# Kernel optimization log

Measured on AMD Instinct MI355X. Metric: run time of the kernel, lower is better.

Reference implementation:

```python
import jax, jax.numpy as jnp
import numpy as np

B, T, DM, H, D = 4, 2048, 1024, 16, 64
INNER = H * D


def setup_inputs() -> dict:
    key = jax.random.key(0)
    ks = jax.random.split(key, 8)
    s = 0.02
    x = jax.random.normal(ks[0], (B, T, DM), dtype=jnp.float32)
    state = jnp.zeros((B, H, D, D), dtype=jnp.float32)
    Wq = jax.random.normal(ks[1], (DM, INNER), dtype=jnp.float32) * s
    Wk = jax.random.normal(ks[2], (DM, INNER), dtype=jnp.float32) * s
    Wv = jax.random.normal(ks[3], (DM, INNER), dtype=jnp.float32) * s
    Wa = jax.random.normal(ks[4], (DM, H), dtype=jnp.float32) * s
    ba = jnp.zeros((H,), dtype=jnp.float32)
    Wb = jax.random.normal(ks[5], (DM, H), dtype=jnp.float32) * s
    bb = jnp.zeros((H,), dtype=jnp.float32)  # beta_init=0.5 -> logit(0.5)=0
    Wo = jax.random.normal(ks[6], (INNER, DM), dtype=jnp.float32) * s
    return {"x": x, "state": state, "Wq": Wq, "Wk": Wk, "Wv": Wv,
            "Wa": Wa, "ba": ba, "Wb": Wb, "bb": bb, "Wo": Wo}


def reference(x, state, Wq, Wk, Wv, Wa, ba, Wb, bb, Wo):
    Bb, Tt, _ = x.shape
    Q = (x @ Wq).reshape(Bb, Tt, H, D)
    K = (x @ Wk).reshape(Bb, Tt, H, D)
    V = (x @ Wv).reshape(Bb, Tt, H, D)
    alpha = jax.nn.sigmoid(x @ Wa + ba)  # (B,T,H) forget gate
    beta = jax.nn.sigmoid(x @ Wb + bb)   # (B,T,H) write gate
    # F.normalize(p=2, dim=-1) with eps=1e-12 clamp on the norm
    K = K / jnp.maximum(jnp.linalg.norm(K, axis=-1, keepdims=True), 1e-12)

    def step(S, inp):
        qt, kt, vt, at, bt = inp  # (B,H,D),(B,H,D),(B,H,D),(B,H),(B,H)
        S = at[..., None, None] * S + bt[..., None, None] * jnp.einsum('bhi,bhj->bhij', vt, kt)
        yt = jnp.einsum('bhij,bhj->bhi', S, qt)
        return S, yt

    xs = (jnp.swapaxes(Q, 0, 1), jnp.swapaxes(K, 0, 1), jnp.swapaxes(V, 0, 1),
          jnp.swapaxes(alpha, 0, 1), jnp.swapaxes(beta, 0, 1))
    S, ys = jax.lax.scan(step, state, xs)  # ys: (T,B,H,D)
    out = jnp.swapaxes(ys, 0, 1).reshape(Bb, Tt, INNER) @ Wo
    return out, S
```

## Files before the change

### kernel.cpp

```cpp
#include <hip/hip_runtime.h>
#include <hip/hip_bf16.h>
#include <math.h>

#define B_SZ   4
#define T_LEN  2048
#define DM     1024
#define NH     16
#define DH     64
#define INNER  1024
#define NROWS  (B_SZ*T_LEN)
#define NQ     (NROWS*INNER)
#define CH     64
#define NCH    (T_LEN/CH)

typedef __bf16 bf16x8 __attribute__((ext_vector_type(8)));
typedef __bf16 bf16x4 __attribute__((ext_vector_type(4)));
typedef float  f32x4  __attribute__((ext_vector_type(4)));
typedef __attribute__((address_space(3))) void*       lds_vp;
typedef const __attribute__((address_space(1))) void* gbl_vp;

__device__ __forceinline__ int swz(int row, int col) {
    return (row << 6) + ((((col >> 3) + (row >> 2)) & 7) << 3) + (col & 7);
}

__global__ __launch_bounds__(256) void wt_cast_transpose(const float* __restrict__ Wq,
                                                         const float* __restrict__ Wk,
                                                         const float* __restrict__ Wv,
                                                         const float* __restrict__ Wo,
                                                         __bf16* __restrict__ WqT,
                                                         __bf16* __restrict__ WkT,
                                                         __bf16* __restrict__ WvT,
                                                         __bf16* __restrict__ WoT) {
    __shared__ float tile[64][65];
    const float* W;
    __bf16* WT;
    if      (blockIdx.z == 0) { W = Wq; WT = WqT; }
    else if (blockIdx.z == 1) { W = Wk; WT = WkT; }
    else if (blockIdx.z == 2) { W = Wv; WT = WvT; }
    else                      { W = Wo; WT = WoT; }

    const int k0 = blockIdx.y * 64, n0 = blockIdx.x * 64;
    const int tr  = threadIdx.x >> 4;
    const int tc4 = (threadIdx.x & 15) * 4;

#pragma unroll
    for (int r = 0; r < 4; r++) {
        const int k = tr + 16 * r;
        const float4 v = *(const float4*)(W + (size_t)(k0 + k) * DM + n0 + tc4);
        tile[k][tc4 + 0] = v.x;
        tile[k][tc4 + 1] = v.y;
        tile[k][tc4 + 2] = v.z;
        tile[k][tc4 + 3] = v.w;
    }
    __syncthreads();
#pragma unroll
    for (int r = 0; r < 4; r++) {
        const int n = tr + 16 * r;
        bf16x4 o;
#pragma unroll
        for (int j = 0; j < 4; j++) o[j] = (__bf16)tile[tc4 + j][n];
        *(bf16x4*)(WT + (size_t)(n0 + n) * DM + k0 + tc4) = o;
    }
}

#define STAGE_STRIDE 24576
#define B_BASE 16384

template <typename CT>
__device__ __forceinline__ void gemm_pipe_body(const __bf16* __restrict__ A,
                                               const __bf16* __restrict__ BT,
                                               CT* __restrict__ C,
                                               int m0, int n0bt, int n0c) {
    __shared__ __align__(16) char lds[3 * STAGE_STRIDE];

    const int tid  = threadIdx.x;
    const int wid  = tid >> 6;
    const int lane = tid & 63;
    const int wm = wid >> 1;
    const int wn = wid & 1;
    const int frow = lane & 15, quad = lane >> 4;

    int offA[8], offB[4];
#pragma unroll
    for (int i = 0; i < 8; ++i) {
        const int ra = wm * 128 + i * 16 + frow;
        offA[i] = ra * 64 + ((quad ^ ((ra >> 1) & 3)) << 4);
    }
#pragma unroll
    for (int j = 0; j < 4; ++j) {
        const int rb = wn * 64 + j * 16 + frow;
        offB[j] = B_BASE + rb * 64 + ((quad ^ ((rb >> 1) & 3)) << 4);
    }

    const int lr = lane >> 2;
    const int cs = ((lane & 3) ^ ((lane >> 3) & 3)) << 3;
    const __bf16* gA[4];
#pragma unroll
    for (int q = 0; q < 4; ++q)
        gA[q] = A + (size_t)(m0 + wid * 64 + q * 16 + lr) * 1024 + cs;
    const __bf16* gB[2];
#pragma unroll
    for (int q = 0; q < 2; ++q)
        gB[q] = BT + (size_t)(n0bt + wid * 32 + q * 16 + lr) * 1024 + cs;

#define STG(t_, b_) do {                                                           \
        _Pragma("unroll")                                                          \
        for (int q_ = 0; q_ < 4; ++q_)                                             \
            __builtin_amdgcn_global_load_lds((gbl_vp)(gA[q_] + (size_t)(t_) * 32), \
                (lds_vp)(lds + (b_) * STAGE_STRIDE + (wid * 64 + q_ * 16) * 64),   \
                16, 0, 0);                                                         \
        _Pragma("unroll")                                                          \
        for (int q_ = 0; q_ < 2; ++q_)                                             \
            __builtin_amdgcn_global_load_lds((gbl_vp)(gB[q_] + (size_t)(t_) * 32), \
                (lds_vp)(lds + (b_) * STAGE_STRIDE + B_BASE + (wid * 32 + q_ * 16) * 64), \
                16, 0, 0);                                                         \
    } while (0)

#define VM6 asm volatile("s_waitcnt vmcnt(6)" ::: "memory")
#define VM0 asm volatile("s_waitcnt vmcnt(0)" ::: "memory")

    f32x4 acc[8][4];
#pragma unroll
    for (int i = 0; i < 8; i++)
#pragma unroll
        for (int j = 0; j < 4; j++) acc[i][j] = (f32x4)0.f;

    STG(0, 0); STG(1, 1);
    VM6;
    asm volatile("s_barrier" ::: "memory");

#define PH(b_, STG_STMT, VM_STMT)                                                  \
    {                                                                              \
        const char* Sb_ = lds + (b_) * STAGE_STRIDE;                               \
        bf16x8 af_[8], bfr_[4];                                                    \
        _Pragma("unroll")                                                          \
        for (int i_ = 0; i_ < 8; ++i_) af_[i_]  = *(const bf16x8*)(Sb_ + offA[i_]);\
        _Pragma("unroll")                                                          \
        for (int j_ = 0; j_ < 4; ++j_) bfr_[j_] = *(const bf16x8*)(Sb_ + offB[j_]);\
        STG_STMT;                                                                  \
        asm volatile("s_barrier" ::: "memory");                                    \
        asm volatile("s_waitcnt lgkmcnt(0)" ::: "memory");                         \
        __builtin_amdgcn_sched_barrier(0);                                         \
        __builtin_amdgcn_s_setprio(1);                                             \
        _Pragma("unroll")                                                          \
        for (int mi_ = 0; mi_ < 8; ++mi_)                                          \
            _Pragma("unroll")                                                      \
            for (int nj_ = 0; nj_ < 4; ++nj_)                                      \
                acc[mi_][nj_] = __builtin_amdgcn_mfma_f32_16x16x32_bf16(           \
                    af_[mi_], bfr_[nj_], acc[mi_][nj_], 0, 0, 0);                  \
        __builtin_amdgcn_s_setprio(0);                                             \
        VM_STMT;                                                                   \
        asm volatile("s_barrier" ::: "memory");                                    \
    }

    for (int u = 0; u < 10; ++u) {
        const int p = 3 * u;
        PH(0, STG(p + 2, 2), VM6);
        PH(1, STG(p + 3, 0), VM6);
        PH(2, STG(p + 4, 1), VM6);
    }
    PH(0, , VM0);
    PH(1, , );

#undef PH
#undef STG
#undef VM6
#undef VM0

    const int cr = quad * 4, cc = frow;
#pragma unroll
    for (int mi = 0; mi < 8; ++mi) {
#pragma unroll
        for (int nj = 0; nj < 4; ++nj) {
            CT* Cp = C + (size_t)(m0 + wm * 128 + mi * 16 + cr) * 1024
                       + n0c + wn * 64 + nj * 16 + cc;
#pragma unroll
            for (int r = 0; r < 4; r++) Cp[(size_t)r * 1024] = (CT)acc[mi][nj][r];
        }
    }
}

__global__ __launch_bounds__(256, 2) void qkv_gemm_8ph(const __bf16* __restrict__ xb,
                                                       const __bf16* __restrict__ BTall,
                                                       __bf16* __restrict__ QKV) {
    const int id = blockIdx.x;
    const int wg = (id & 7) * 96 + (id >> 3);
    const int mt = wg / 24, nt = wg % 24;
    const int mat = nt >> 3;
    gemm_pipe_body<__bf16>(xb, BTall, QKV + (size_t)mat * NQ,
                           mt * 256, nt * 128, (nt & 7) * 128);
}

__global__ __launch_bounds__(256, 2) void out_gemm_8ph(const __bf16* __restrict__ Yb,
                                                       const __bf16* __restrict__ WoT,
                                                       float* __restrict__ Cout) {
    const int id = blockIdx.x;
    const int wg = (id & 7) * 32 + (id >> 3);
    const int mt = wg >> 3, nt = wg & 7;
    gemm_pipe_body<float>(Yb, WoT, Cout, mt * 256, nt * 128, nt * 128);
}

#define WGS 1032
#define LAS 40
__global__ __launch_bounds__(256) void gates_fused(const float* __restrict__ x,
                                                   const float* __restrict__ Wa,
                                                   const float* __restrict__ ba,
                                                   const float* __restrict__ Wb,
                                                   const float* __restrict__ bb,
                                                   float* __restrict__ AlphaT,
                                                   float* __restrict__ BetaT,
                                                   __bf16* __restrict__ xb) {
    __shared__ __align__(16) __bf16 lWg[32 * WGS];
    __shared__ __align__(16) __bf16 lA[64 * LAS];

    const int tid = threadIdx.x;
    const int wid = tid >> 6, lane = tid & 63;
    const int quad = lane >> 4, frow = lane & 15;
    const int m0 = blockIdx.x * 64;

    {
        const int kbase = tid * 4;
#pragma unroll
        for (int j = 0; j < 4; j++) {
            const int k = kbase + j;
            const float4* war = (const float4*)(Wa + (size_t)k * NH);
            const float4* wbr = (const float4*)(Wb + (size_t)k * NH);
#pragma unroll
            for (int q = 0; q < 4; q++) {
                const float4 a = war[q], bq = wbr[q];
                lWg[(q * 4 + 0) * WGS + k] = (__bf16)a.x;
                lWg[(q * 4 + 1) * WGS + k] = (__bf16)a.y;
                lWg[(q * 4 + 2) * WGS + k] = (__bf16)a.z;
                lWg[(q * 4 + 3) * WGS + k] = (__bf16)a.w;
                lWg[(16 + q * 4 + 0) * WGS + k] = (__bf16)bq.x;
                lWg[(16 + q * 4 + 1) * WGS + k] = (__bf16)bq.y;
                lWg[(16 + q * 4 + 2) * WGS + k] = (__bf16)bq.z;
                lWg[(16 + q * 4 + 3) * WGS + k] = (__bf16)bq.w;
            }
        }
    }
    const float bias_a = ba[frow];
    const float bias_b = bb[frow];

    const int rrow = tid >> 2;
    const int rk   = (tid & 3) * 8;
    const float* xrow = x + (size_t)(m0 + rrow) * DM + rk;
    float4 c0 = *(const float4*)(xrow + 0);
    float4 c1 = *(const float4*)(xrow + 4);

    f32x4 acc[2];
    acc[0] = (f32x4)0.f; acc[1] = (f32x4)0.f;

    for (int k0 = 0; k0 < DM; k0 += 32) {
        __syncthreads();
        bf16x8 xv;
        xv[0] = (__bf16)c0.x; xv[1] = (__bf16)c0.y; xv[2] = (__bf16)c0.z; xv[3] = (__bf16)c0.w;
        xv[4] = (__bf16)c1.x; xv[5] = (__bf16)c1.y; xv[6] = (__bf16)c1.z; xv[7] = (__bf16)c1.w;
        *(bf16x8*)&lA[rrow * LAS + rk] = xv;
        *(bf16x8*)(xb + (size_t)(m0 + rrow) * DM + k0 + rk) = xv;
        if (k0 + 32 < DM) {
            c0 = *(const float4*)(xrow + k0 + 32);
            c1 = *(const float4*)(xrow + k0 + 36);
        }
        __syncthreads();
        const bf16x8 af = *(const bf16x8*)&lA[(wid * 16 + frow) * LAS + quad * 8];
#pragma unroll
        for (int ct = 0; ct < 2; ct++) {
            const bf16x8 bf = *(const bf16x8*)&lWg[(ct * 16 + frow) * WGS + k0 + quad * 8];
            acc[ct] = __builtin_amdgcn_mfma_f32_16x16x32_bf16(af, bf, acc[ct], 0, 0, 0);
        }
    }

#pragma unroll
    for (int ct = 0; ct < 2; ct++) {
        const float bias = (ct == 0) ? bias_a : bias_b;
        float* dst = (ct == 0) ? AlphaT : BetaT;
#pragma unroll
        for (int r = 0; r < 4; r++) {
            const int row = m0 + wid * 16 + quad * 4 + r;
            const float s = acc[ct][r] + bias;
            dst[(size_t)frow * NROWS + row] = 1.f / (1.f + __expf(-s));
        }
    }
}

__global__ __launch_bounds__(256) void chunk_ds(const __bf16* __restrict__ Q,
                                                const __bf16* __restrict__ K,
                                                __bf16* __restrict__ V,
                                                const float* __restrict__ AlphaT,
                                                const float* __restrict__ BetaT,
                                                float* __restrict__ Dec,
                                                float* __restrict__ DS,
                                                float* __restrict__ ExpT) {
    __shared__ __align__(16) __bf16 Qb[64 * 64];
    __shared__ __align__(16) __bf16 Kb[64 * 64];
    __shared__ __align__(16) __bf16 KTs[64 * 64];
    __shared__ __align__(16) __bf16 VTb[64 * 64];
    __shared__ __align__(16) __bf16 Ab[64 * 64];
    __shared__ float sla[64], sb[64], swd[64];

    const int blk = blockIdx.x;
    const int c = blk & 31, h = (blk >> 5) & 15, b = blk >> 9;
    const int t0 = c * CH;
    const int tid = threadIdx.x;
    const int wid = tid >> 6, lane = tid & 63;
    const size_t rowbase = ((size_t)(b * T_LEN + t0) * NH + h) * DH;

    const int srow = tid >> 3;
    const int scol = (tid & 7) * 8;
    bf16x8 q8[2], k8[2], v8[2];
#pragma unroll
    for (int r = 0; r < 2; r++) {
        const size_t g = rowbase + (size_t)(srow + 32 * r) * INNER + scol;
        q8[r] = *(const bf16x8*)(Q + g);
        k8[r] = *(const bf16x8*)(K + g);
        v8[r] = *(const bf16x8*)(V + g);
    }

    if (tid < 64) {
        const int t = tid;
        const size_t gaT = (size_t)h * NROWS + b * T_LEN + t0 + t;
        const float a  = AlphaT[gaT];
        const float bt = BetaT[gaT];
        float xx = logf(a);
#pragma unroll
        for (int off = 1; off < 64; off <<= 1) {
            const float y = __shfl_up(xx, off, 64);
            if (t >= off) xx += y;
        }
        const float la63 = __shfl(xx, 63, 64);
        sla[t] = xx;
        sb[t]  = bt;
        swd[t] = bt * __expf(la63 - xx);
        ExpT[gaT] = __expf(xx);
        if (t == 63) Dec[(size_t)(b * NH + h) * NCH + c] = __expf(la63);
    }
    __syncthreads();

#pragma unroll
    for (int r = 0; r < 2; r++) {
        const int row = srow + 32 * r;
        float kf[8];
        float ss = 0.f;
#pragma unroll
        for (int j = 0; j < 8; j++) { kf[j] = (float)k8[r][j]; ss += kf[j] * kf[j]; }
        ss += __shfl_xor(ss, 1, 64);
        ss += __shfl_xor(ss, 2, 64);
        ss += __shfl_xor(ss, 4, 64);
        const float scale = 1.f / fmaxf(sqrtf(ss), 1e-12f);
        const float w = swd[row];
        bf16x8 kn8;
#pragma unroll
        for (int j = 0; j < 8; j++) {
            const float kn = kf[j] * scale;
            kn8[j] = (__bf16)kn;
            KTs[swz(scol + j, row)] = (__bf16)(w * kn);
            VTb[swz(scol + j, row)] = v8[r][j];
        }
        *(bf16x8*)&Qb[swz(row, scol)] = q8[r];
        *(bf16x8*)&Kb[swz(row, scol)] = kn8;
    }
    __syncthreads();

    const int quad = lane >> 4;
    const int frow = lane & 15;
    const int tw = wid * 16;

    f32x4 accG[4];
#pragma unroll
    for (int i = 0; i < 4; i++) accG[i] = (f32x4)0.f;
#pragma unroll
    for (int ks = 0; ks < 2; ks++) {
        const int ko = quad * 8 + 32 * ks;
        const bf16x8 aq = *(const bf16x8*)&Qb[swz(tw + frow, ko)];
#pragma unroll
        for (int st = 0; st < 4; st++) {
            const bf16x8 bk = *(const bf16x8*)&Kb[swz(st * 16 + frow, ko)];
            accG[st] = __builtin_amdgcn_mfma_f32_16x16x32_bf16(aq, bk, accG[st], 0, 0, 0);
        }
    }
#pragma unroll
    for (int st = 0; st < 4; st++) {
#pragma unroll
        for (int r = 0; r < 4; r++) {
            const int t = tw + quad * 4 + r;
            const int s = st * 16 + frow;
            const float av = (s <= t) ? __expf(sla[t] - sla[s]) * sb[s] * accG[st][r] : 0.f;
            Ab[swz(t, s)] = (__bf16)av;
        }
    }
    __syncthreads();

    f32x4 accY[4], accD[4];
#pragma unroll
    for (int i = 0; i < 4; i++) { accY[i] = (f32x4)0.f; accD[i] = (f32x4)0.f; }
#pragma unroll
    for (int ks = 0; ks < 2; ks++) {
        const int ko = quad * 8 + 32 * ks;
        const bf16x8 aA = *(const bf16x8*)&Ab[swz(tw + frow, ko)];
        const bf16x8 aV = *(const bf16x8*)&VTb[swz(tw + frow, ko)];
#pragma unroll
        for (int jt = 0; jt < 4; jt++) {
            const bf16x8 bv = *(const bf16x8*)&VTb[swz(jt * 16 + frow, ko)];
            const bf16x8 bk = *(const bf16x8*)&KTs[swz(jt * 16 + frow, ko)];
            accY[jt] = __builtin_amdgcn_mfma_f32_16x16x32_bf16(aA, bv, accY[jt], 0, 0, 0);
            accD[jt] = __builtin_amdgcn_mfma_f32_16x16x32_bf16(aV, bk, accD[jt], 0, 0, 0);
        }
    }
#pragma unroll
    for (int jt = 0; jt < 4; jt++) {
#pragma unroll
        for (int r = 0; r < 4; r++) {
            const int row = tw + quad * 4 + r;
            const size_t g = rowbase + (size_t)row * INNER + jt * 16 + frow;
            V[g]  = (__bf16)accY[jt][r];
            DS[g] = accD[jt][r];
        }
    }
}

__global__ __launch_bounds__(256) void chunk_state(const float* __restrict__ DS,
                                                   const float* __restrict__ Dec,
                                                   const float* __restrict__ state_in,
                                                   float* __restrict__ state_out,
                                                   __bf16* __restrict__ ScB) {
    const int blk = blockIdx.x;
    const int b = blk >> 4, h = blk & 15;
    const int tid = threadIdx.x;
    const int w = tid >> 6;
    const int l = tid & 63;

    float S[16];
    {
        const float* st = state_in + ((size_t)(b * NH + h) * DH + l) * DH + 16 * w;
#pragma unroll
        for (int j4 = 0; j4 < 4; j4++)
            *(float4*)&S[4 * j4] = *(const float4*)(st + 4 * j4);
    }

    for (int c = 0; c < NCH; c++) {
        const int t0 = c * CH;
        const float decay = Dec[(size_t)(b * NH + h) * NCH + c];
        const size_t off = ((size_t)(b * T_LEN + t0 + l) * NH + h) * DH + 16 * w;
        const float* ds = DS + off;
        __bf16* sc = ScB + off;
        float4 dv[4];
#pragma unroll
        for (int j4 = 0; j4 < 4; j4++) dv[j4] = *(const float4*)(ds + 4 * j4);
#pragma unroll
        for (int j4 = 0; j4 < 4; j4++) {
            bf16x4 o;
            o[0] = (__bf16)S[4 * j4 + 0]; o[1] = (__bf16)S[4 * j4 + 1];
            o[2] = (__bf16)S[4 * j4 + 2]; o[3] = (__bf16)S[4 * j4 + 3];
            *(bf16x4*)(sc + 4 * j4) = o;
        }
#pragma unroll
        for (int j4 = 0; j4 < 4; j4++) {
            S[4 * j4 + 0] = decay * S[4 * j4 + 0] + dv[j4].x;
            S[4 * j4 + 1] = decay * S[4 * j4 + 1] + dv[j4].y;
            S[4 * j4 + 2] = decay * S[4 * j4 + 2] + dv[j4].z;
            S[4 * j4 + 3] = decay * S[4 * j4 + 3] + dv[j4].w;
        }
    }

    float* so = state_out + ((size_t)(b * NH + h) * DH + l) * DH + 16 * w;
#pragma unroll
    for (int j4 = 0; j4 < 4; j4++)
        *(float4*)(so + 4 * j4) = *(const float4*)&S[4 * j4];
}

__global__ __launch_bounds__(256) void chunk_y(const __bf16* __restrict__ Q,
                                               const __bf16* __restrict__ ScB,
                                               __bf16* __restrict__ Yb,
                                               const float* __restrict__ ExpT) {
    __shared__ __align__(16) __bf16 Qb[64 * 64];
    __shared__ __align__(16) __bf16 Scb[64 * 64];
    __shared__ float sexp[64];

    const int blk = blockIdx.x;
    const int c = blk & 31, h = (blk >> 5) & 15, b = blk >> 9;
    const int t0 = c * CH;
    const int tid = threadIdx.x;
    const int wid = tid >> 6, lane = tid & 63;
    const size_t rowbase = ((size_t)(b * T_LEN + t0) * NH + h) * DH;

    const int srow = tid >> 3;
    const int scol = (tid & 7) * 8;
    bf16x8 q8[2], s8[2];
#pragma unroll
    for (int r = 0; r < 2; r++) {
        const size_t g = rowbase + (size_t)(srow + 32 * r) * INNER + scol;
        q8[r] = *(const bf16x8*)(Q + g);
        s8[r] = *(const bf16x8*)(ScB + g);
    }

    if (tid < 64)
        sexp[tid] = ExpT[(size_t)h * NROWS + b * T_LEN + t0 + tid];

#pragma unroll
    for (int r = 0; r < 2; r++) {
        *(bf16x8*)&Qb[swz(srow + 32 * r, scol)]  = q8[r];
        *(bf16x8*)&Scb[swz(srow + 32 * r, scol)] = s8[r];
    }
    __syncthreads();

    const int quad = lane >> 4;
    const int frow = lane & 15;
    const int tw = wid * 16;

    f32x4 accU[4];
#pragma unroll
    for (int i = 0; i < 4; i++) accU[i] = (f32x4)0.f;
#pragma unroll
    for (int ks = 0; ks < 2; ks++) {
        const int ko = quad * 8 + 32 * ks;
        const bf16x8 aq = *(const bf16x8*)&Qb[swz(tw + frow, ko)];
#pragma unroll
        for (int it = 0; it < 4; it++) {
            const bf16x8 bs = *(const bf16x8*)&Scb[swz(it * 16 + frow, ko)];
            accU[it] = __builtin_amdgcn_mfma_f32_16x16x32_bf16(aq, bs, accU[it], 0, 0, 0);
        }
    }

#pragma unroll
    for (int it = 0; it < 4; it++) {
#pragma unroll
        for (int r = 0; r < 4; r++) {
            const int t = tw + quad * 4 + r;
            const size_t g = rowbase + (size_t)t * INNER + it * 16 + frow;
            Yb[g] = (__bf16)(sexp[t] * accU[it][r] + (float)Yb[g]);
        }
    }
}

extern "C" void kernel_launch(void* const* d_in, const int* in_sizes, int n_in,
                              void* d_out, int out_size, void* d_ws, size_t ws_size,
                              hipStream_t stream) {
    const float* x     = (const float*)d_in[0];
    const float* state = (const float*)d_in[1];
    const float* Wq    = (const float*)d_in[2];
    const float* Wk    = (const float*)d_in[3];
    const float* Wv    = (const float*)d_in[4];
    const float* Wa    = (const float*)d_in[5];
    const float* ba    = (const float*)d_in[6];
    const float* Wb    = (const float*)d_in[7];
    const float* bb    = (const float*)d_in[8];
    const float* Wo    = (const float*)d_in[9];

    __bf16* Qb    = (__bf16*)d_ws;
    __bf16* Kbf   = Qb + (size_t)NQ;
    __bf16* Vbf   = Kbf + (size_t)NQ;
    float*  DS    = (float*)(Vbf + (size_t)NQ);
    float*  AlphaT= DS + (size_t)NQ;
    float*  BetaT = AlphaT + (size_t)NROWS * NH;
    float*  ExpT  = BetaT + (size_t)NROWS * NH;
    float*  Dec   = ExpT + (size_t)NROWS * NH;
    __bf16* xb    = (__bf16*)(Dec + (size_t)B_SZ * NH * NCH);
    __bf16* ScB   = xb;
    __bf16* WqT   = xb + (size_t)NQ;
    __bf16* WkT   = WqT + (size_t)DM * INNER;
    __bf16* WvT   = WkT + (size_t)DM * INNER;
    __bf16* WoT   = WvT + (size_t)DM * INNER;

    float* out  = (float*)d_out;
    float* Sout = out + (size_t)NQ;

    wt_cast_transpose<<<dim3(16, 16, 4), 256, 0, stream>>>(Wq, Wk, Wv, Wo,
                                                           WqT, WkT, WvT, WoT);
    gates_fused<<<NROWS / 64, 256, 0, stream>>>(x, Wa, ba, Wb, bb,
                                                AlphaT, BetaT, xb);
    qkv_gemm_8ph<<<768, 256, 0, stream>>>(xb, WqT, Qb);
    chunk_ds<<<B_SZ * NH * NCH, 256, 0, stream>>>(Qb, Kbf, Vbf, AlphaT, BetaT,
                                                  Dec, DS, ExpT);
    chunk_state<<<B_SZ * NH, 256, 0, stream>>>(DS, Dec, state, Sout, ScB);
    chunk_y<<<B_SZ * NH * NCH, 256, 0, stream>>>(Qb, ScB, Vbf, ExpT);
    out_gemm_8ph<<<256, 256, 0, stream>>>(Vbf, WoT, out);
}
```

Before: 278.6 us.

## Fuse chunk state recurrence with inter-chunk output into one kernel

Merges the sequential chunk_state scan and the chunk_y inter-chunk output GEMM into a single state_y kernel. The running state stays in registers as an MFMA B operand, so the per-chunk bf16 state snapshots no longer round-trip through global memory and one launch is removed. The DS product in chunk_ds is changed to a transposed layout (K^T V order) so each thread can read its state column. Parallelism rises from 64 to 256 blocks, but each block walks all chunks serially, and the DS and Y accesses are strided scalar loads and stores that may coalesce poorly.

```diff
diff --git a/kernel.cpp b/kernel.cpp
--- a/kernel.cpp
+++ b/kernel.cpp
@@ -398,13 +398,12 @@
     for (int ks = 0; ks < 2; ks++) {
         const int ko = quad * 8 + 32 * ks;
         const bf16x8 aA = *(const bf16x8*)&Ab[swz(tw + frow, ko)];
-        const bf16x8 aV = *(const bf16x8*)&VTb[swz(tw + frow, ko)];
+        const bf16x8 aK = *(const bf16x8*)&KTs[swz(tw + frow, ko)];
 #pragma unroll
         for (int jt = 0; jt < 4; jt++) {
             const bf16x8 bv = *(const bf16x8*)&VTb[swz(jt * 16 + frow, ko)];
-            const bf16x8 bk = *(const bf16x8*)&KTs[swz(jt * 16 + frow, ko)];
             accY[jt] = __builtin_amdgcn_mfma_f32_16x16x32_bf16(aA, bv, accY[jt], 0, 0, 0);
-            accD[jt] = __builtin_amdgcn_mfma_f32_16x16x32_bf16(aV, bk, accD[jt], 0, 0, 0);
+            accD[jt] = __builtin_amdgcn_mfma_f32_16x16x32_bf16(aK, bv, accD[jt], 0, 0, 0);
         }
     }
 #pragma unroll
@@ -419,117 +418,84 @@
     }
 }
 
-__global__ __launch_bounds__(256) void chunk_state(const float* __restrict__ DS,
-                                                   const float* __restrict__ Dec,
-                                                   const float* __restrict__ state_in,
-                                                   float* __restrict__ state_out,
-                                                   __bf16* __restrict__ ScB) {
+__global__ __launch_bounds__(256) void state_y(const __bf16* __restrict__ Q,
+                                               const float* __restrict__ DS,
+                                               const float* __restrict__ Dec,
+                                               const float* __restrict__ ExpT,
+                                               const float* __restrict__ state_in,
+                                               float* __restrict__ state_out,
+                                               __bf16* __restrict__ Yb) {
     const int blk = blockIdx.x;
-    const int b = blk >> 4, h = blk & 15;
+    const int b = blk >> 6, h = (blk >> 2) & 15, iq = blk & 3;
     const int tid = threadIdx.x;
-    const int w = tid >> 6;
-    const int l = tid & 63;
-
-    float S[16];
+    const int wid = tid >> 6, lane = tid & 63;
+    const int frow = lane & 15, quad = lane >> 4;
+    const int tw = wid * 16;
+    const int i = iq * 16 + frow;
+
+    float S[2][8];
     {
-        const float* st = state_in + ((size_t)(b * NH + h) * DH + l) * DH + 16 * w;
-#pragma unroll
-        for (int j4 = 0; j4 < 4; j4++)
-            *(float4*)&S[4 * j4] = *(const float4*)(st + 4 * j4);
-    }
-
+        const float* st = state_in + ((size_t)((b * NH + h) * DH) + i) * DH;
+#pragma unroll
+        for (int ks = 0; ks < 2; ks++) {
+            const int j0 = 32 * ks + quad * 8;
+            const float4 a = *(const float4*)(st + j0);
+            const float4 d = *(const float4*)(st + j0 + 4);
+            S[ks][0] = a.x; S[ks][1] = a.y; S[ks][2] = a.z; S[ks][3] = a.w;
+            S[ks][4] = d.x; S[ks][5] = d.y; S[ks][6] = d.z; S[ks][7] = d.w;
+        }
+    }
+
+    const size_t bh = (size_t)(b * NH + h);
+#pragma unroll 2
     for (int c = 0; c < NCH; c++) {
         const int t0 = c * CH;
-        const float decay = Dec[(size_t)(b * NH + h) * NCH + c];
-        const size_t off = ((size_t)(b * T_LEN + t0 + l) * NH + h) * DH + 16 * w;
-        const float* ds = DS + off;
-        __bf16* sc = ScB + off;
-        float4 dv[4];
-#pragma unroll
-        for (int j4 = 0; j4 < 4; j4++) dv[j4] = *(const float4*)(ds + 4 * j4);
-#pragma unroll
-        for (int j4 = 0; j4 < 4; j4++) {
-            bf16x4 o;
-            o[0] = (__bf16)S[4 * j4 + 0]; o[1] = (__bf16)S[4 * j4 + 1];
-            o[2] = (__bf16)S[4 * j4 + 2]; o[3] = (__bf16)S[4 * j4 + 3];
-            *(bf16x4*)(sc + 4 * j4) = o;
-        }
-#pragma unroll
-        for (int j4 = 0; j4 < 4; j4++) {
-            S[4 * j4 + 0] = decay * S[4 * j4 + 0] + dv[j4].x;
-            S[4 * j4 + 1] = decay * S[4 * j4 + 1] + dv[j4].y;
-            S[4 * j4 + 2] = decay * S[4 * j4 + 2] + dv[j4].z;
-            S[4 * j4 + 3] = decay * S[4 * j4 + 3] + dv[j4].w;
-        }
-    }
-
-    float* so = state_out + ((size_t)(b * NH + h) * DH + l) * DH + 16 * w;
-#pragma unroll
-    for (int j4 = 0; j4 < 4; j4++)
-        *(float4*)(so + 4 * j4) = *(const float4*)&S[4 * j4];
-}
-
-__global__ __launch_bounds__(256) void chunk_y(const __bf16* __restrict__ Q,
-                                               const __bf16* __restrict__ ScB,
-                                               __bf16* __restrict__ Yb,
-                                               const float* __restrict__ ExpT) {
-    __shared__ __align__(16) __bf16 Qb[64 * 64];
-    __shared__ __align__(16) __bf16 Scb[64 * 64];
-    __shared__ float sexp[64];
-
-    const int blk = blockIdx.x;
-    const int c = blk & 31, h = (blk >> 5) & 15, b = blk >> 9;
-    const int t0 = c * CH;
-    const int tid = threadIdx.x;
-    const int wid = tid >> 6, lane = tid & 63;
-    const size_t rowbase = ((size_t)(b * T_LEN + t0) * NH + h) * DH;
-
-    const int srow = tid >> 3;
-    const int scol = (tid & 7) * 8;
-    bf16x8 q8[2], s8[2];
-#pragma unroll
-    for (int r = 0; r < 2; r++) {
-        const size_t g = rowbase + (size_t)(srow + 32 * r) * INNER + scol;
-        q8[r] = *(const bf16x8*)(Q + g);
-        s8[r] = *(const bf16x8*)(ScB + g);
-    }
-
-    if (tid < 64)
-        sexp[tid] = ExpT[(size_t)h * NROWS + b * T_LEN + t0 + tid];
-
-#pragma unroll
-    for (int r = 0; r < 2; r++) {
-        *(bf16x8*)&Qb[swz(srow + 32 * r, scol)]  = q8[r];
-        *(bf16x8*)&Scb[swz(srow + 32 * r, scol)] = s8[r];
-    }
-    __syncthreads();
-
-    const int quad = lane >> 4;
-    const int frow = lane & 15;
-    const int tw = wid * 16;
-
-    f32x4 accU[4];
-#pragma unroll
-    for (int i = 0; i < 4; i++) accU[i] = (f32x4)0.f;
-#pragma unroll
-    for (int ks = 0; ks < 2; ks++) {
-        const int ko = quad * 8 + 32 * ks;
-        const bf16x8 aq = *(const bf16x8*)&Qb[swz(tw + frow, ko)];
-#pragma unroll
-        for (int it = 0; it < 4; it++) {
-            const bf16x8 bs = *(const bf16x8*)&Scb[swz(it * 16 + frow, ko)];
-            accU[it] = __builtin_amdgcn_mfma_f32_16x16x32_bf16(aq, bs, accU[it], 0, 0, 0);
-        }
-    }
-
-#pragma unroll
-    for (int it = 0; it < 4; it++) {
+        const size_t rowbase = ((size_t)(b * T_LEN + t0) * NH + h) * DH;
+        const float decay = Dec[bh * NCH + c];
+
+        const bf16x8 aq0 = *(const bf16x8*)(Q + rowbase + (size_t)(tw + frow) * INNER + quad * 8);
+        const bf16x8 aq1 = *(const bf16x8*)(Q + rowbase + (size_t)(tw + frow) * INNER + 32 + quad * 8);
+
+        float ds[2][8];
+#pragma unroll
+        for (int ks = 0; ks < 2; ks++) {
+            const int j0 = 32 * ks + quad * 8;
+#pragma unroll
+            for (int e = 0; e < 8; e++)
+                ds[ks][e] = DS[rowbase + (size_t)(j0 + e) * INNER + i];
+        }
+
+        bf16x8 bs0, bs1;
+#pragma unroll
+        for (int e = 0; e < 8; e++) { bs0[e] = (__bf16)S[0][e]; bs1[e] = (__bf16)S[1][e]; }
+
+        f32x4 acc = (f32x4)0.f;
+        acc = __builtin_amdgcn_mfma_f32_16x16x32_bf16(aq0, bs0, acc, 0, 0, 0);
+        acc = __builtin_amdgcn_mfma_f32_16x16x32_bf16(aq1, bs1, acc, 0, 0, 0);
+
+#pragma unroll
+        for (int ks = 0; ks < 2; ks++)
+#pragma unroll
+            for (int e = 0; e < 8; e++)
+                S[ks][e] = decay * S[ks][e] + ds[ks][e];
+
 #pragma unroll
         for (int r = 0; r < 4; r++) {
             const int t = tw + quad * 4 + r;
-            const size_t g = rowbase + (size_t)t * INNER + it * 16 + frow;
-            Yb[g] = (__bf16)(sexp[t] * accU[it][r] + (float)Yb[g]);
-        }
+            const float ee = ExpT[(size_t)h * NROWS + b * T_LEN + t0 + t];
+            __bf16* yp = Yb + rowbase + (size_t)t * INNER + i;
+            *yp = (__bf16)(ee * acc[r] + (float)*yp);
+        }
+    }
+
+    float* so = state_out + ((size_t)((b * NH + h) * DH) + i) * DH;
+#pragma unroll
+    for (int ks = 0; ks < 2; ks++) {
+        const int j0 = 32 * ks + quad * 8;
+        const float4 v0 = {S[ks][0], S[ks][1], S[ks][2], S[ks][3]};
+        const float4 v1 = {S[ks][4], S[ks][5], S[ks][6], S[ks][7]};
+        *(float4*)(so + j0)     = v0;
+        *(float4*)(so + j0 + 4) = v1;
     }
 }
 
@@ -556,7 +522,6 @@
     float*  ExpT  = BetaT + (size_t)NROWS * NH;
     float*  Dec   = ExpT + (size_t)NROWS * NH;
     __bf16* xb    = (__bf16*)(Dec + (size_t)B_SZ * NH * NCH);
-    __bf16* ScB   = xb;
     __bf16* WqT   = xb + (size_t)NQ;
     __bf16* WkT   = WqT + (size_t)DM * INNER;
     __bf16* WvT   = WkT + (size_t)DM * INNER;
@@ -572,7 +537,7 @@
     qkv_gemm_8ph<<<768, 256, 0, stream>>>(xb, WqT, Qb);
     chunk_ds<<<B_SZ * NH * NCH, 256, 0, stream>>>(Qb, Kbf, Vbf, AlphaT, BetaT,
                                                   Dec, DS, ExpT);
-    chunk_state<<<B_SZ * NH, 256, 0, stream>>>(DS, Dec, state, Sout, ScB);
-    chunk_y<<<B_SZ * NH * NCH, 256, 0, stream>>>(Qb, ScB, Vbf, ExpT);
+    state_y<<<B_SZ * NH * 4, 256, 0, stream>>>(Qb, DS, Dec, ExpT, state,
+                                               Sout, Vbf);
     out_gemm_8ph<<<256, 256, 0, stream>>>(Vbf, WoT, out);
 }
```

Result: faster. 262.8 us (-5.7%).
